# Performance work log

Measured on AMD Instinct MI355X. Metric: run time of the kernel, lower is better.

Reference implementation:

```python
import jax, jax.numpy as jnp
import numpy as np

EPS = 1e-8  # torch F.cosine_similarity default eps


def setup_inputs() -> dict:
    key = jax.random.key(0)
    k1, k2 = jax.random.split(key)
    B_times_n, L, C = 512, 256, 256
    x1 = jax.random.normal(k1, (B_times_n, L, C), dtype=jnp.float32)
    x2 = jax.random.normal(k2, (B_times_n, L, C), dtype=jnp.float32)
    return {"x1": x1, "x2": x2, "n": 8}


def reference(x1, x2, n):
    # x1, x2: [batch_size*n, L, C] -> flatten each sample to a vector
    N = x1.shape[0]
    a = x1.reshape(N, -1)
    b = x2.reshape(N, -1)
    dot = jnp.sum(a * b, axis=-1)                      # [N]
    denom = jnp.linalg.norm(a, axis=-1) * jnp.linalg.norm(b, axis=-1)
    cos = dot / jnp.maximum(denom, EPS)                # per-sample cosine sim
    # segmented mean over consecutive groups of n -> [batch_size]
    return cos.reshape(-1, n).mean(axis=-1)
```

## Files before the change

### kernel.cpp

```cpp
#include <hip/hip_runtime.h>

static constexpr int LC   = 256 * 256;
static constexpr int V4   = LC / 4;
static constexpr int TPB  = 1024;

__global__ __launch_bounds__(TPB) void cos_per_sample_kernel(
    const float* __restrict__ x1, const float* __restrict__ x2,
    float* __restrict__ cos_ws)
{
    const size_t base = (size_t)blockIdx.x * LC;
    const float4* a4 = reinterpret_cast<const float4*>(x1 + base);
    const float4* b4 = reinterpret_cast<const float4*>(x2 + base);

    double dot = 0.0, sa = 0.0, sb = 0.0;

    #pragma unroll 4
    for (int i = threadIdx.x; i < V4; i += TPB) {
        float4 a = a4[i];
        float4 b = b4[i];
        float pd = a.x * b.x + a.y * b.y + a.z * b.z + a.w * b.w;
        float pa = a.x * a.x + a.y * a.y + a.z * a.z + a.w * a.w;
        float pb = b.x * b.x + b.y * b.y + b.z * b.z + b.w * b.w;
        dot += (double)pd;
        sa  += (double)pa;
        sb  += (double)pb;
    }

    #pragma unroll
    for (int off = 32; off > 0; off >>= 1) {
        dot += __shfl_down(dot, off, 64);
        sa  += __shfl_down(sa,  off, 64);
        sb  += __shfl_down(sb,  off, 64);
    }

    __shared__ double s[3][TPB / 64];
    const int wave = threadIdx.x >> 6;
    if ((threadIdx.x & 63) == 0) {
        s[0][wave] = dot;
        s[1][wave] = sa;
        s[2][wave] = sb;
    }
    __syncthreads();

    if (threadIdx.x == 0) {
        double D = 0.0, A = 0.0, B = 0.0;
        #pragma unroll
        for (int w = 0; w < TPB / 64; ++w) {
            D += s[0][w];
            A += s[1][w];
            B += s[2][w];
        }
        double denom = sqrt(A) * sqrt(B);
        denom = fmax(denom, 1e-8);
        cos_ws[blockIdx.x] = (float)(D / denom);
    }
}

__global__ void segmented_mean_kernel(const float* __restrict__ cos_ws,
                                      float* __restrict__ out,
                                      int n, int groups)
{
    int g = blockIdx.x * blockDim.x + threadIdx.x;
    if (g < groups) {
        float s = 0.0f;
        for (int j = 0; j < n; ++j) s += cos_ws[g * n + j];
        out[g] = s / (float)n;
    }
}

extern "C" void kernel_launch(void* const* d_in, const int* in_sizes, int n_in,
                              void* d_out, int out_size, void* d_ws, size_t ws_size,
                              hipStream_t stream)
{
    const float* x1 = (const float*)d_in[0];
    const float* x2 = (const float*)d_in[1];
    float* out = (float*)d_out;
    float* ws  = (float*)d_ws;

    const int N      = in_sizes[0] / LC;
    const int groups = out_size;
    const int n      = N / groups;

    cos_per_sample_kernel<<<N, TPB, 0, stream>>>(x1, x2, ws);

    int mtpb = 64;
    int mblocks = (groups + mtpb - 1) / mtpb;
    segmented_mean_kernel<<<mblocks, mtpb, 0, stream>>>(ws, out, n, groups);
}
```

Before: 274.4 us.

## Split each sample across four blocks with fp32 partials and single-block finalize

Each sample's reduction is split across four 256-thread blocks that write partial dot and norm sums, and a single-block finalize kernel combines them, computes the cosine and does the segmented mean. Accumulation switches from double to float with two independent accumulator sets and a fully unrolled loop. The goal is more blocks and memory-level parallelism for this bandwidth-bound reduction and removal of fp64 conversion overhead. The cost is reduced accumulation precision and a finalize kernel limited to 512 samples.

```diff
diff --git a/kernel.cpp b/kernel.cpp
--- a/kernel.cpp
+++ b/kernel.cpp
@@ -1,30 +1,42 @@
 #include <hip/hip_runtime.h>
 
-static constexpr int LC   = 256 * 256;
-static constexpr int V4   = LC / 4;
-static constexpr int TPB  = 1024;
+static constexpr int LC  = 256 * 256;
+static constexpr int BPS = 4;
+static constexpr int TPB = 256;
+static constexpr int CHUNK4 = (LC / 4) / BPS;
+static constexpr int ITERS  = CHUNK4 / TPB;
 
-__global__ __launch_bounds__(TPB) void cos_per_sample_kernel(
+__global__ __launch_bounds__(TPB, 8) void cos_partial_kernel(
     const float* __restrict__ x1, const float* __restrict__ x2,
-    float* __restrict__ cos_ws)
+    float* __restrict__ ws)
 {
-    const size_t base = (size_t)blockIdx.x * LC;
-    const float4* a4 = reinterpret_cast<const float4*>(x1 + base);
-    const float4* b4 = reinterpret_cast<const float4*>(x2 + base);
+    const size_t base4 = (size_t)blockIdx.x * CHUNK4;
+    const float4* a4 = reinterpret_cast<const float4*>(x1) + base4;
+    const float4* b4 = reinterpret_cast<const float4*>(x2) + base4;
 
-    double dot = 0.0, sa = 0.0, sb = 0.0;
+    float dot0 = 0.f, dot1 = 0.f;
+    float sa0 = 0.f, sa1 = 0.f;
+    float sb0 = 0.f, sb1 = 0.f;
 
-    #pragma unroll 4
-    for (int i = threadIdx.x; i < V4; i += TPB) {
-        float4 a = a4[i];
-        float4 b = b4[i];
-        float pd = a.x * b.x + a.y * b.y + a.z * b.z + a.w * b.w;
-        float pa = a.x * a.x + a.y * a.y + a.z * a.z + a.w * a.w;
-        float pb = b.x * b.x + b.y * b.y + b.z * b.z + b.w * b.w;
-        dot += (double)pd;
-        sa  += (double)pa;
-        sb  += (double)pb;
+    #pragma unroll
+    for (int it = 0; it < ITERS; it += 2) {
+        float4 a0 = a4[(size_t)it * TPB + threadIdx.x];
+        float4 b0 = b4[(size_t)it * TPB + threadIdx.x];
+        float4 a1 = a4[(size_t)(it + 1) * TPB + threadIdx.x];
+        float4 b1 = b4[(size_t)(it + 1) * TPB + threadIdx.x];
+
+        dot0 += a0.x * b0.x + a0.y * b0.y + a0.z * b0.z + a0.w * b0.w;
+        sa0  += a0.x * a0.x + a0.y * a0.y + a0.z * a0.z + a0.w * a0.w;
+        sb0  += b0.x * b0.x + b0.y * b0.y + b0.z * b0.z + b0.w * b0.w;
+
+        dot1 += a1.x * b1.x + a1.y * b1.y + a1.z * b1.z + a1.w * b1.w;
+        sa1  += a1.x * a1.x + a1.y * a1.y + a1.z * a1.z + a1.w * a1.w;
+        sb1  += b1.x * b1.x + b1.y * b1.y + b1.z * b1.z + b1.w * b1.w;
     }
+
+    float dot = dot0 + dot1;
+    float sa  = sa0 + sa1;
+    float sb  = sb0 + sb1;
 
     #pragma unroll
     for (int off = 32; off > 0; off >>= 1) {
@@ -33,7 +45,7 @@
         sb  += __shfl_down(sb,  off, 64);
     }
 
-    __shared__ double s[3][TPB / 64];
+    __shared__ float s[3][TPB / 64];
     const int wave = threadIdx.x >> 6;
     if ((threadIdx.x & 63) == 0) {
         s[0][wave] = dot;
@@ -43,28 +55,44 @@
     __syncthreads();
 
     if (threadIdx.x == 0) {
-        double D = 0.0, A = 0.0, B = 0.0;
+        float D = 0.f, A = 0.f, B = 0.f;
         #pragma unroll
         for (int w = 0; w < TPB / 64; ++w) {
             D += s[0][w];
             A += s[1][w];
             B += s[2][w];
         }
-        double denom = sqrt(A) * sqrt(B);
-        denom = fmax(denom, 1e-8);
-        cos_ws[blockIdx.x] = (float)(D / denom);
+        float* o = ws + (size_t)blockIdx.x * 4;
+        o[0] = D;
+        o[1] = A;
+        o[2] = B;
     }
 }
 
-__global__ void segmented_mean_kernel(const float* __restrict__ cos_ws,
-                                      float* __restrict__ out,
-                                      int n, int groups)
+__global__ __launch_bounds__(512) void cos_finalize_kernel(
+    const float* __restrict__ ws, float* __restrict__ out,
+    int n_samples, int n, int groups)
 {
-    int g = blockIdx.x * blockDim.x + threadIdx.x;
-    if (g < groups) {
-        float s = 0.0f;
-        for (int j = 0; j < n; ++j) s += cos_ws[g * n + j];
-        out[g] = s / (float)n;
+    __shared__ float cos_s[512];
+    const int s = threadIdx.x;
+    if (s < n_samples) {
+        float D = 0.f, A = 0.f, B = 0.f;
+        #pragma unroll
+        for (int q = 0; q < BPS; ++q) {
+            const float* p = ws + (size_t)(s * BPS + q) * 4;
+            D += p[0];
+            A += p[1];
+            B += p[2];
+        }
+        float denom = sqrtf(A) * sqrtf(B);
+        denom = fmaxf(denom, 1e-8f);
+        cos_s[s] = D / denom;
+    }
+    __syncthreads();
+    if (s < groups) {
+        float m = 0.f;
+        for (int j = 0; j < n; ++j) m += cos_s[s * n + j];
+        out[s] = m / (float)n;
     }
 }
 
@@ -77,13 +105,11 @@
     float* out = (float*)d_out;
     float* ws  = (float*)d_ws;
 
-    const int N      = in_sizes[0] / LC;
-    const int groups = out_size;
-    const int n      = N / groups;
+    const int n_samples = in_sizes[0] / LC;
+    const int groups    = out_size;
+    const int n         = n_samples / groups;
+    const int n_blocks  = n_samples * BPS;
 
-    cos_per_sample_kernel<<<N, TPB, 0, stream>>>(x1, x2, ws);
-
-    int mtpb = 64;
-    int mblocks = (groups + mtpb - 1) / mtpb;
-    segmented_mean_kernel<<<mblocks, mtpb, 0, stream>>>(ws, out, n, groups);
+    cos_partial_kernel<<<n_blocks, TPB, 0, stream>>>(x1, x2, ws);
+    cos_finalize_kernel<<<1, 512, 0, stream>>>(ws, out, n_samples, n, groups);
 }
```

After: 272.9 us. Within noise of the previous version (-0.6%).
